# Kernel tuning notes

Measured on AMD Instinct MI355X. Metric: run time of the kernel, lower is better.

## Reference

```python
import jax, jax.numpy as jnp
import numpy as np

HEADS = 12
DIM_HEAD = 64
SCALE = DIM_HEAD ** -0.5

def setup_inputs() -> dict:
    key = jax.random.key(0)
    k1, k2, k3, k4 = jax.random.split(key, 4)
    dim, inner = 768, HEADS * DIM_HEAD
    x = jax.random.normal(k1, (4, 2048, dim), dtype=jnp.float32)
    w_qkv = jax.random.normal(k2, (dim, 3 * inner), dtype=jnp.float32) * (dim ** -0.5)
    w_out = jax.random.normal(k3, (inner, dim), dtype=jnp.float32) * (inner ** -0.5)
    b_out = jax.random.normal(k4, (dim,), dtype=jnp.float32) * 0.02
    return {"x": x, "w_qkv": w_qkv, "w_out": w_out, "b_out": b_out}

def reference(x, w_qkv, w_out, b_out):
    B, N, _ = x.shape
    qkv = jnp.einsum('bnd,de->bne', x, w_qkv)  # [B,N,3*inner]
    q, k, v = jnp.split(qkv, 3, axis=-1)
    # b n (h d) -> b h n d
    split_heads = lambda t: t.reshape(B, N, HEADS, DIM_HEAD).transpose(0, 2, 1, 3)
    q, k, v = split_heads(q), split_heads(k), split_heads(v)
    dots = jnp.einsum('bhnd,bhmd->bhnm', q, k) * SCALE  # [B,H,N,N]
    attn = jax.nn.softmax(dots, axis=-1)
    out = jnp.einsum('bhnm,bhmd->bhnd', attn, v)
    out = out.transpose(0, 2, 1, 3).reshape(B, N, HEADS * DIM_HEAD)  # b h n d -> b n (h d)
    return jnp.einsum('bne,ed->bnd', out, w_out) + b_out
```

## Files before the change

### kernel.cpp

```cpp
#include <hip/hip_runtime.h>
#include <stdint.h>

typedef unsigned short ushort_t;
typedef __attribute__((ext_vector_type(8))) short short8;
typedef __attribute__((ext_vector_type(4))) float f32x4;
typedef __attribute__((ext_vector_type(2))) uint32_t u32x2;

#define BATCH 4
#define SEQ 2048
#define DMODEL 768
#define NH 12
#define HD 64
#define QKV3 2304
#define NHEADS 48
#define SCALE_Q 0.18033688011112042f

__device__ __forceinline__ ushort_t f2bf(float f) {
    union { float f; uint32_t u; } v; v.f = f;
    uint32_t u = v.u;
    u += 0x7FFF + ((u >> 16) & 1);
    return (ushort_t)(u >> 16);
}

__device__ __forceinline__ uint32_t pack_bf16(float a, float b) {
#if __has_builtin(__builtin_amdgcn_cvt_pk_bf16_f32)
    typedef __attribute__((ext_vector_type(2))) __bf16 bf16x2;
    bf16x2 r = __builtin_amdgcn_cvt_pk_bf16_f32(a, b);
    return __builtin_bit_cast(uint32_t, r);
#else
    return ((uint32_t)f2bf(b) << 16) | (uint32_t)f2bf(a);
#endif
}

typedef __attribute__((address_space(1))) uint32_t as1_u32;
typedef __attribute__((address_space(3))) uint32_t as3_u32;
__device__ __forceinline__ void async16(void* lds, const void* gsrc) {
    __builtin_amdgcn_global_load_lds((as1_u32*)gsrc, (as3_u32*)lds, 16, 0, 0);
}

__device__ __forceinline__ void wait_vm_lgkm0() {
    __builtin_amdgcn_s_waitcnt(0x0070);
}
__device__ __forceinline__ void wait_vm4_lgkm0() {
    __builtin_amdgcn_s_waitcnt(0x0074);
}

__device__ __forceinline__ void swap32(uint32_t& a, uint32_t& b) {
    asm("v_permlane32_swap_b32 %0, %1" : "+v"(a), "+v"(b));
}
__device__ __forceinline__ void swap16(uint32_t& a, uint32_t& b) {
    asm("v_permlane16_swap_b32 %0, %1" : "+v"(a), "+v"(b));
}

__global__ __launch_bounds__(256) void cvt_bf16(
    const float* __restrict__ in, ushort_t* __restrict__ out) {
    int i = blockIdx.x * 256 + threadIdx.x;
    float4 v = *(const float4*)(in + (size_t)i * 4);
    ushort4 o; o.x = f2bf(v.x); o.y = f2bf(v.y); o.z = f2bf(v.z); o.w = f2bf(v.w);
    *(ushort4*)(out + (size_t)i * 4) = o;
}

__global__ __launch_bounds__(256) void transpose_f32_bf16(
    const float* __restrict__ in, ushort_t* __restrict__ out, int R, int C) {
    __shared__ ushort_t t[64][72];
    const int tid = threadIdx.x;
    const int r0 = blockIdx.y * 64, c0 = blockIdx.x * 64;
#pragma unroll
    for (int i = 0; i < 4; i++) {
        int idx = tid + i * 256;
        int row = idx >> 4, c4 = (idx & 15) * 4;
        float4 v = *(const float4*)(in + (size_t)(r0 + row) * C + c0 + c4);
        ushort4 o; o.x = f2bf(v.x); o.y = f2bf(v.y); o.z = f2bf(v.z); o.w = f2bf(v.w);
        *(ushort4*)&t[row][c4] = o;
    }
    __syncthreads();
#pragma unroll
    for (int i = 0; i < 2; i++) {
        int idx = tid + i * 256;
        int oc = idx >> 3, g8 = (idx & 7) * 8;
        ushort_t tmp[8];
#pragma unroll
        for (int e = 0; e < 8; e++) tmp[e] = t[g8 + e][oc];
        *(short8*)(out + (size_t)(c0 + oc) * R + r0 + g8) = *(const short8*)tmp;
    }
}

__global__ __launch_bounds__(256, 2) void gemm_qkv(
    const ushort_t* __restrict__ A, const ushort_t* __restrict__ B,
    ushort_t* __restrict__ qkv, ushort_t* __restrict__ vT) {
    __shared__ ushort_t As[128 * 64];
    __shared__ ushort_t Bs[128 * 64];

    const int tid = threadIdx.x;
    const int m0 = blockIdx.y * 128, n0 = blockIdx.x * 128;
    const int lane = tid & 63, w = tid >> 6;
    const int wm = w >> 1, wn = w & 1;
    const int l16 = lane & 15, quad = lane >> 4;

    f32x4 acc[4][4];
#pragma unroll
    for (int i = 0; i < 4; i++)
#pragma unroll
        for (int j = 0; j < 4; j++) acc[i][j] = (f32x4){0.f, 0.f, 0.f, 0.f};

    int srow[4], scol[4];
#pragma unroll
    for (int j = 0; j < 4; j++) {
        int s = j * 256 + tid;
        srow[j] = s >> 3;
        scol[j] = ((s & 7) ^ (srow[j] & 7)) * 8;
    }
    const int swz0 = (quad ^ (l16 & 7)) * 8;
    const int swz1 = ((4 + quad) ^ (l16 & 7)) * 8;

    for (int kt = 0; kt < DMODEL; kt += 64) {
#pragma unroll
        for (int j = 0; j < 4; j++) {
            async16(&As[(j * 256 + w * 64) * 8],
                    A + (size_t)(m0 + srow[j]) * DMODEL + kt + scol[j]);
            async16(&Bs[(j * 256 + w * 64) * 8],
                    B + (size_t)(n0 + srow[j]) * DMODEL + kt + scol[j]);
        }
        wait_vm_lgkm0();
        __syncthreads();

        short8 a[4][2], b[4][2];
#pragma unroll
        for (int mi = 0; mi < 4; mi++) {
            int r = (wm * 64 + mi * 16 + l16) * 64;
            a[mi][0] = *(const short8*)&As[r + swz0];
            a[mi][1] = *(const short8*)&As[r + swz1];
        }
#pragma unroll
        for (int ni = 0; ni < 4; ni++) {
            int r = (wn * 64 + ni * 16 + l16) * 64;
            b[ni][0] = *(const short8*)&Bs[r + swz0];
            b[ni][1] = *(const short8*)&Bs[r + swz1];
        }
#pragma unroll
        for (int kk = 0; kk < 2; kk++)
#pragma unroll
            for (int mi = 0; mi < 4; mi++)
#pragma unroll
                for (int ni = 0; ni < 4; ni++)
                    acc[mi][ni] = __builtin_amdgcn_mfma_f32_16x16x32_bf16(
                        a[mi][kk], b[ni][kk], acc[mi][ni], 0, 0, 0);
        __syncthreads();
    }

#pragma unroll
    for (int ni = 0; ni < 4; ni++) {
        int nbase = n0 + wn * 64 + ni * 16;
        int which = nbase / DMODEL;
        int rem = nbase - which * DMODEL;
        int h = rem >> 6;
        int d = (rem & 63) + l16;
        if (which == 2) {
#pragma unroll
            for (int mi = 0; mi < 4; mi++) {
                int mg = m0 + wm * 64 + mi * 16 + quad * 4;
                int b_ = mg >> 11, ns = mg & 2047;
                u32x2 pk = {pack_bf16(acc[mi][ni][0], acc[mi][ni][1]),
                            pack_bf16(acc[mi][ni][2], acc[mi][ni][3])};
                *(u32x2*)(vT + ((size_t)(b_ * NH + h) * HD + d) * SEQ + ns) = pk;
            }
        } else {
            float scale = (which == 0) ? SCALE_Q : 1.0f;
#pragma unroll
            for (int mi = 0; mi < 4; mi++) {
#pragma unroll
                for (int r = 0; r < 4; r++) {
                    int mg = m0 + wm * 64 + mi * 16 + quad * 4 + r;
                    int b_ = mg >> 11, ns = mg & 2047;
                    size_t dst = (((size_t)(which * BATCH + b_) * NH + h) * SEQ + ns) * HD + d;
                    qkv[dst] = f2bf(acc[mi][ni][r] * scale);
                }
            }
        }
    }
}

__global__ __launch_bounds__(256, 3) void attn(
    const ushort_t* __restrict__ qkv, const ushort_t* __restrict__ vT,
    ushort_t* __restrict__ ao) {
    __shared__ ushort_t smem[24576];

    const int tid = threadIdx.x;
    const int bid = blockIdx.x;
    const int i = bid >> 3;
    const int bh = (bid & 7) + 8 * (i % 6);
    const int qt = i / 6;
    const int lane = tid & 63, w = tid >> 6;
    const int l16 = lane & 15, quad = lane >> 4;
    const int qh7 = l16 & 7;

    const ushort_t* qh = qkv + (size_t)bh * (SEQ * HD);
    const ushort_t* kh = qkv + (size_t)(NHEADS + bh) * (SEQ * HD);
    const ushort_t* vh = vT + (size_t)bh * (HD * SEQ);

    short8 aq[2][2];
#pragma unroll
    for (int mi = 0; mi < 2; mi++)
#pragma unroll
        for (int kk = 0; kk < 2; kk++) {
            int row = qt * 128 + w * 32 + mi * 16 + l16;
            aq[mi][kk] = *(const short8*)(qh + (size_t)row * HD + kk * 32 + quad * 8);
        }

    short8 ones8;
#pragma unroll
    for (int j = 0; j < 8; j++) ones8[j] = (short)0x3F80;

    f32x4 acc_l[2];
    f32x4 O[4][2];
#pragma unroll
    for (int mi = 0; mi < 2; mi++) acc_l[mi] = (f32x4){0.f, 0.f, 0.f, 0.f};
#pragma unroll
    for (int nd = 0; nd < 4; nd++)
#pragma unroll
        for (int mi = 0; mi < 2; mi++) O[nd][mi] = (f32x4){0.f, 0.f, 0.f, 0.f};

    int srow[2], scol[2];
#pragma unroll
    for (int j = 0; j < 2; j++) {
        int s = j * 256 + tid;
        srow[j] = s >> 3;
        scol[j] = ((s & 7) ^ (srow[j] & 7)) * 8;
    }
    const int swz0 = (quad ^ qh7) * 8;
    const int swz1 = ((4 + quad) ^ qh7) * 8;

    auto stage = [&](int t, int buf) {
        int nb = buf * 8192, j1 = t * 64;
#pragma unroll
        for (int j = 0; j < 2; j++) {
            async16(&smem[nb + (j * 256 + w * 64) * 8],
                    kh + (size_t)(j1 + srow[j]) * HD + scol[j]);
            async16(&smem[nb + 4096 + (j * 256 + w * 64) * 8],
                    vh + (size_t)srow[j] * SEQ + j1 + scol[j]);
        }
    };

    auto compute = [&](const ushort_t* Ks) {
        const ushort_t* Vs = Ks + 4096;
#pragma unroll
        for (int p = 0; p < 2; p++) {
            uint32_t pkv[2][2][2];
#pragma unroll
            for (int sub = 0; sub < 2; sub++) {
                const int ni = p * 2 + sub;
                int r = (ni * 16 + l16) * 64;
                short8 ak0 = *(const short8*)&Ks[r + swz0];
                short8 ak1 = *(const short8*)&Ks[r + swz1];
#pragma unroll
                for (int mi = 0; mi < 2; mi++) {
                    f32x4 s = __builtin_amdgcn_mfma_f32_16x16x32_bf16(
                        ak0, aq[mi][0], (f32x4){0.f, 0.f, 0.f, 0.f}, 0, 0, 0);
                    s = __builtin_amdgcn_mfma_f32_16x16x32_bf16(
                        ak1, aq[mi][1], s, 0, 0, 0);
                    f32x4 pr;
#pragma unroll
                    for (int rr = 0; rr < 4; rr++)
                        pr[rr] = __builtin_amdgcn_exp2f(s[rr]);
                    pkv[sub][mi][0] = pack_bf16(pr[0], pr[1]);
                    pkv[sub][mi][1] = pack_bf16(pr[2], pr[3]);
                }
            }
            short8 bp32[2];
#pragma unroll
            for (int mi = 0; mi < 2; mi++) {
                uint32_t x0 = pkv[0][mi][0], y0 = pkv[1][mi][0];
                uint32_t x1 = pkv[0][mi][1], y1 = pkv[1][mi][1];
                swap32(x0, y0); swap16(x0, y0);
                swap32(x1, y1); swap16(x1, y1);
                union { short8 s; uint32_t u[4]; } bu;
                bu.u[0] = x0; bu.u[1] = x1; bu.u[2] = y0; bu.u[3] = y1;
                bp32[mi] = bu.s;
            }
            __builtin_amdgcn_s_setprio(1);
#pragma unroll
            for (int mi = 0; mi < 2; mi++)
                acc_l[mi] = __builtin_amdgcn_mfma_f32_16x16x32_bf16(
                    ones8, bp32[mi], acc_l[mi], 0, 0, 0);
#pragma unroll
            for (int nd = 0; nd < 4; nd++) {
                int vrow = nd * 16 + l16;
                short8 av = *(const short8*)&Vs[vrow * 64 +
                                                (((p * 4 + quad) ^ qh7) * 8)];
#pragma unroll
                for (int mi = 0; mi < 2; mi++)
                    O[nd][mi] = __builtin_amdgcn_mfma_f32_16x16x32_bf16(
                        av, bp32[mi], O[nd][mi], 0, 0, 0);
            }
            __builtin_amdgcn_s_setprio(0);
        }
    };

    stage(0, 0);
    stage(1, 1);

    const int NT = SEQ / 64;
    for (int t = 0; t < NT - 1; t++) {
        wait_vm4_lgkm0();
        __builtin_amdgcn_s_barrier();
        if (t + 2 < NT) stage(t + 2, (t + 2) % 3);
        compute(smem + (t % 3) * 8192);
    }
    wait_vm_lgkm0();
    __builtin_amdgcn_s_barrier();
    compute(smem + ((NT - 1) % 3) * 8192);

    float inv[2];
#pragma unroll
    for (int mi = 0; mi < 2; mi++)
        inv[mi] = __builtin_amdgcn_rcpf(acc_l[mi][0]);
    __syncthreads();
    ushort_t* Lt = smem;
#pragma unroll
    for (int mi = 0; mi < 2; mi++)
#pragma unroll
        for (int nd = 0; nd < 4; nd++) {
            int row = w * 32 + mi * 16 + l16;
            int col = nd * 16 + quad * 4;
            uint32_t d0 = pack_bf16(O[nd][mi][0] * inv[mi], O[nd][mi][1] * inv[mi]);
            uint32_t d1 = pack_bf16(O[nd][mi][2] * inv[mi], O[nd][mi][3] * inv[mi]);
            *(u32x2*)&Lt[row * 72 + col] = (u32x2){d0, d1};
        }
    __syncthreads();

    const int b_ = bh / NH, h = bh % NH;
#pragma unroll
    for (int i2 = 0; i2 < 4; i2++) {
        int idx = tid + i2 * 256;
        int row = idx >> 3, c8 = (idx & 7) * 8;
        short8 vv = *(const short8*)&Lt[row * 72 + c8];
        *(short8*)(ao + ((size_t)(b_ * SEQ + qt * 128 + row)) * DMODEL +
                   h * HD + c8) = vv;
    }
}

__global__ __launch_bounds__(256, 2) void gemm_out(
    const ushort_t* __restrict__ A, const ushort_t* __restrict__ B,
    const float* __restrict__ bias, float* __restrict__ out) {
    __shared__ ushort_t As[128 * 64];
    __shared__ ushort_t Bs[128 * 64];

    const int tid = threadIdx.x;
    const int m0 = blockIdx.y * 128, n0 = blockIdx.x * 128;
    const int lane = tid & 63, w = tid >> 6;
    const int wm = w >> 1, wn = w & 1;
    const int l16 = lane & 15, quad = lane >> 4;

    f32x4 acc[4][4];
#pragma unroll
    for (int i = 0; i < 4; i++)
#pragma unroll
        for (int j = 0; j < 4; j++) acc[i][j] = (f32x4){0.f, 0.f, 0.f, 0.f};

    int srow[4], scol[4];
#pragma unroll
    for (int j = 0; j < 4; j++) {
        int s = j * 256 + tid;
        srow[j] = s >> 3;
        scol[j] = ((s & 7) ^ (srow[j] & 7)) * 8;
    }
    const int swz0 = (quad ^ (l16 & 7)) * 8;
    const int swz1 = ((4 + quad) ^ (l16 & 7)) * 8;

    for (int kt = 0; kt < DMODEL; kt += 64) {
#pragma unroll
        for (int j = 0; j < 4; j++) {
            async16(&As[(j * 256 + w * 64) * 8],
                    A + (size_t)(m0 + srow[j]) * DMODEL + kt + scol[j]);
            async16(&Bs[(j * 256 + w * 64) * 8],
                    B + (size_t)(n0 + srow[j]) * DMODEL + kt + scol[j]);
        }
        wait_vm_lgkm0();
        __syncthreads();

        short8 a[4][2], b[4][2];
#pragma unroll
        for (int mi = 0; mi < 4; mi++) {
            int r = (wm * 64 + mi * 16 + l16) * 64;
            a[mi][0] = *(const short8*)&As[r + swz0];
            a[mi][1] = *(const short8*)&As[r + swz1];
        }
#pragma unroll
        for (int ni = 0; ni < 4; ni++) {
            int r = (wn * 64 + ni * 16 + l16) * 64;
            b[ni][0] = *(const short8*)&Bs[r + swz0];
            b[ni][1] = *(const short8*)&Bs[r + swz1];
        }
#pragma unroll
        for (int kk = 0; kk < 2; kk++)
#pragma unroll
            for (int mi = 0; mi < 4; mi++)
#pragma unroll
                for (int ni = 0; ni < 4; ni++)
                    acc[mi][ni] = __builtin_amdgcn_mfma_f32_16x16x32_bf16(
                        a[mi][kk], b[ni][kk], acc[mi][ni], 0, 0, 0);
        __syncthreads();
    }

#pragma unroll
    for (int ni = 0; ni < 4; ni++) {
        int ng = n0 + wn * 64 + ni * 16 + l16;
        float bv = bias[ng];
#pragma unroll
        for (int mi = 0; mi < 4; mi++) {
#pragma unroll
            for (int r = 0; r < 4; r++) {
                int mg = m0 + wm * 64 + mi * 16 + quad * 4 + r;
                out[(size_t)mg * DMODEL + ng] = acc[mi][ni][r] + bv;
            }
        }
    }
}

extern "C" void kernel_launch(void* const* d_in, const int* in_sizes, int n_in,
                              void* d_out, int out_size, void* d_ws, size_t ws_size,
                              hipStream_t stream) {
    const float* x     = (const float*)d_in[0];
    const float* w_qkv = (const float*)d_in[1];
    const float* w_out = (const float*)d_in[2];
    const float* b_out = (const float*)d_in[3];
    float* out = (float*)d_out;

    ushort_t* xb  = (ushort_t*)d_ws;
    ushort_t* wqT = xb  + (size_t)8192 * 768;
    ushort_t* woT = wqT + (size_t)QKV3 * 768;
    ushort_t* qkv = woT + (size_t)768 * 768;
    ushort_t* vT  = qkv + (size_t)3 * NHEADS * SEQ * HD;
    ushort_t* ao  = vT  + (size_t)NHEADS * HD * SEQ;

    cvt_bf16<<<dim3((8192 * 768) / 4 / 256), 256, 0, stream>>>(x, xb);
    transpose_f32_bf16<<<dim3(QKV3 / 64, DMODEL / 64), 256, 0, stream>>>(
        w_qkv, wqT, DMODEL, QKV3);
    transpose_f32_bf16<<<dim3(DMODEL / 64, DMODEL / 64), 256, 0, stream>>>(
        w_out, woT, DMODEL, DMODEL);

    gemm_qkv<<<dim3(QKV3 / 128, (BATCH * SEQ) / 128), 256, 0, stream>>>(
        xb, wqT, qkv, vT);

    attn<<<dim3(NHEADS * (SEQ / 128)), 256, 0, stream>>>(qkv, vT, ao);

    gemm_out<<<dim3(DMODEL / 128, (BATCH * SEQ) / 128), 256, 0, stream>>>(
        ao, woT, b_out, out);
}
```

Measured before the change: 216.1 us.

## Double-buffer LDS tiles in QKV and output GEMMs to overlap loads with MFMA

Result: no change. 214.9 us (-0.6%).

```diff
diff --git a/kernel.cpp b/kernel.cpp
--- a/kernel.cpp
+++ b/kernel.cpp
@@ -88,8 +88,8 @@
 __global__ __launch_bounds__(256, 2) void gemm_qkv(
     const ushort_t* __restrict__ A, const ushort_t* __restrict__ B,
     ushort_t* __restrict__ qkv, ushort_t* __restrict__ vT) {
-    __shared__ ushort_t As[128 * 64];
-    __shared__ ushort_t Bs[128 * 64];
+    __shared__ ushort_t As[2][128 * 64];
+    __shared__ ushort_t Bs[2][128 * 64];
 
     const int tid = threadIdx.x;
     const int m0 = blockIdx.y * 128, n0 = blockIdx.x * 128;
@@ -113,29 +113,37 @@
     const int swz0 = (quad ^ (l16 & 7)) * 8;
     const int swz1 = ((4 + quad) ^ (l16 & 7)) * 8;
 
-    for (int kt = 0; kt < DMODEL; kt += 64) {
+    auto stage = [&](int kt, int buf) {
 #pragma unroll
         for (int j = 0; j < 4; j++) {
-            async16(&As[(j * 256 + w * 64) * 8],
-                    A + (size_t)(m0 + srow[j]) * DMODEL + kt + scol[j]);
-            async16(&Bs[(j * 256 + w * 64) * 8],
-                    B + (size_t)(n0 + srow[j]) * DMODEL + kt + scol[j]);
-        }
+            async16(&As[buf][(j * 256 + w * 64) * 8],
+                    A + (size_t)(m0 + srow[j]) * DMODEL + kt * 64 + scol[j]);
+            async16(&Bs[buf][(j * 256 + w * 64) * 8],
+                    B + (size_t)(n0 + srow[j]) * DMODEL + kt * 64 + scol[j]);
+        }
+    };
+
+    stage(0, 0);
+    const int NKT = DMODEL / 64;
+    for (int t = 0; t < NKT; t++) {
         wait_vm_lgkm0();
-        __syncthreads();
-
+        __builtin_amdgcn_s_barrier();
+        if (t + 1 < NKT) stage(t + 1, (t + 1) & 1);
+
+        const ushort_t* Asb = As[t & 1];
+        const ushort_t* Bsb = Bs[t & 1];
         short8 a[4][2], b[4][2];
 #pragma unroll
         for (int mi = 0; mi < 4; mi++) {
             int r = (wm * 64 + mi * 16 + l16) * 64;
-            a[mi][0] = *(const short8*)&As[r + swz0];
-            a[mi][1] = *(const short8*)&As[r + swz1];
+            a[mi][0] = *(const short8*)&Asb[r + swz0];
+            a[mi][1] = *(const short8*)&Asb[r + swz1];
         }
 #pragma unroll
         for (int ni = 0; ni < 4; ni++) {
             int r = (wn * 64 + ni * 16 + l16) * 64;
-            b[ni][0] = *(const short8*)&Bs[r + swz0];
-            b[ni][1] = *(const short8*)&Bs[r + swz1];
+            b[ni][0] = *(const short8*)&Bsb[r + swz0];
+            b[ni][1] = *(const short8*)&Bsb[r + swz1];
         }
 #pragma unroll
         for (int kk = 0; kk < 2; kk++)
@@ -145,7 +153,6 @@
                 for (int ni = 0; ni < 4; ni++)
                     acc[mi][ni] = __builtin_amdgcn_mfma_f32_16x16x32_bf16(
                         a[mi][kk], b[ni][kk], acc[mi][ni], 0, 0, 0);
-        __syncthreads();
     }
 
 #pragma unroll
@@ -342,8 +349,8 @@
 __global__ __launch_bounds__(256, 2) void gemm_out(
     const ushort_t* __restrict__ A, const ushort_t* __restrict__ B,
     const float* __restrict__ bias, float* __restrict__ out) {
-    __shared__ ushort_t As[128 * 64];
-    __shared__ ushort_t Bs[128 * 64];
+    __shared__ ushort_t As[2][128 * 64];
+    __shared__ ushort_t Bs[2][128 * 64];
 
     const int tid = threadIdx.x;
     const int m0 = blockIdx.y * 128, n0 = blockIdx.x * 128;
@@ -367,29 +374,37 @@
     const int swz0 = (quad ^ (l16 & 7)) * 8;
     const int swz1 = ((4 + quad) ^ (l16 & 7)) * 8;
 
-    for (int kt = 0; kt < DMODEL; kt += 64) {
+    auto stage = [&](int kt, int buf) {
 #pragma unroll
         for (int j = 0; j < 4; j++) {
-            async16(&As[(j * 256 + w * 64) * 8],
-                    A + (size_t)(m0 + srow[j]) * DMODEL + kt + scol[j]);
-            async16(&Bs[(j * 256 + w * 64) * 8],
-                    B + (size_t)(n0 + srow[j]) * DMODEL + kt + scol[j]);
-        }
+            async16(&As[buf][(j * 256 + w * 64) * 8],
+                    A + (size_t)(m0 + srow[j]) * DMODEL + kt * 64 + scol[j]);
+            async16(&Bs[buf][(j * 256 + w * 64) * 8],
+                    B + (size_t)(n0 + srow[j]) * DMODEL + kt * 64 + scol[j]);
+        }
+    };
+
+    stage(0, 0);
+    const int NKT = DMODEL / 64;
+    for (int t = 0; t < NKT; t++) {
         wait_vm_lgkm0();
-        __syncthreads();
-
+        __builtin_amdgcn_s_barrier();
+        if (t + 1 < NKT) stage(t + 1, (t + 1) & 1);
+
+        const ushort_t* Asb = As[t & 1];
+        const ushort_t* Bsb = Bs[t & 1];
         short8 a[4][2], b[4][2];
 #pragma unroll
         for (int mi = 0; mi < 4; mi++) {
             int r = (wm * 64 + mi * 16 + l16) * 64;
-            a[mi][0] = *(const short8*)&As[r + swz0];
-            a[mi][1] = *(const short8*)&As[r + swz1];
+            a[mi][0] = *(const short8*)&Asb[r + swz0];
+            a[mi][1] = *(const short8*)&Asb[r + swz1];
         }
 #pragma unroll
         for (int ni = 0; ni < 4; ni++) {
             int r = (wn * 64 + ni * 16 + l16) * 64;
-            b[ni][0] = *(const short8*)&Bs[r + swz0];
-            b[ni][1] = *(const short8*)&Bs[r + swz1];
+            b[ni][0] = *(const short8*)&Bsb[r + swz0];
+            b[ni][1] = *(const short8*)&Bsb[r + swz1];
         }
 #pragma unroll
         for (int kk = 0; kk < 2; kk++)
@@ -399,7 +414,6 @@
                 for (int ni = 0; ni < 4; ni++)
                     acc[mi][ni] = __builtin_amdgcn_mfma_f32_16x16x32_bf16(
                         a[mi][kk], b[ni][kk], acc[mi][ni], 0, 0, 0);
-        __syncthreads();
     }
 
 #pragma unroll
```
